# Kernel tuning notes

Hardware: AMD Instinct MI355X
Metric: run time of the kernel (lower is better)

## Reference

```python
import jax, jax.numpy as jnp
import numpy as np

N_NODES = 50000
N_EDGES = 800000
D_NODE = 128
D_EDGE = 128
D_OUT = 256
HID = 256


def setup_inputs() -> dict:
    key = jax.random.key(0)
    ks = jax.random.split(key, 10)
    s1 = 1.0 / np.sqrt(D_NODE + D_EDGE)
    s2 = 1.0 / np.sqrt(HID)
    s3 = 1.0 / np.sqrt(D_NODE + HID)
    return {
        "x": jax.random.normal(ks[0], (N_NODES, D_NODE), dtype=jnp.float32),
        "edge_index": jax.random.randint(ks[1], (2, N_EDGES), 0, N_NODES, dtype=jnp.int64),
        "edge_attr": jax.random.normal(ks[2], (N_EDGES, D_EDGE), dtype=jnp.float32),
        "u": jax.random.normal(ks[3], (1, 64), dtype=jnp.float32),
        "batch": jnp.zeros((N_NODES,), dtype=jnp.int64),
        "w1a": jax.random.normal(ks[4], (D_NODE + D_EDGE, HID), dtype=jnp.float32) * s1,
        "b1a": jnp.zeros((HID,), dtype=jnp.float32),
        "w1b": jax.random.normal(ks[5], (HID, HID), dtype=jnp.float32) * s2,
        "b1b": jnp.zeros((HID,), dtype=jnp.float32),
        "w2a": jax.random.normal(ks[6], (D_NODE + HID, HID), dtype=jnp.float32) * s3,
        "b2a": jnp.zeros((HID,), dtype=jnp.float32),
        "w2b": jax.random.normal(ks[7], (HID, D_OUT), dtype=jnp.float32) * s2,
        "b2b": jnp.zeros((D_OUT,), dtype=jnp.float32),
    }


def reference(x, edge_index, edge_attr, u, batch, w1a, b1a, w1b, b1b, w2a, b2a, w2b, b2b):
    row, col = edge_index[0], edge_index[1]
    # edge-wise MLP: [E, D_NODE + D_EDGE] -> 256 -> 256
    h = jnp.concatenate([x[row], edge_attr], axis=1)
    h = jax.nn.elu(h @ w1a + b1a) @ w1b + b1b  # [E, 256]
    # scatter_mean over destination nodes (dim_size = N)
    n = x.shape[0]
    sums = jax.ops.segment_sum(h, col, num_segments=n)  # [N, 256]
    cnt = jax.ops.segment_sum(jnp.ones((h.shape[0],), h.dtype), col, num_segments=n)
    mean = sums / jnp.maximum(cnt, 1.0)[:, None]
    # node-wise MLP: [N, D_NODE + 256] -> 256 -> D_OUT
    z = jnp.concatenate([x, mean], axis=1)
    return jax.nn.elu(z @ w2a + b2a) @ w2b + b2b
```

## Files before the change

### kernel.cpp

```cpp
#include <hip/hip_runtime.h>
#include <hip/hip_bf16.h>

#define N_NODES 50000
#define N_EDGES 800000

typedef short s16x8 __attribute__((ext_vector_type(8)));
typedef short s16x4 __attribute__((ext_vector_type(4)));
typedef float f32x4 __attribute__((ext_vector_type(4)));

__device__ __forceinline__ unsigned short f2bf(float f) {
    union { float f; unsigned u; } v; v.f = f;
    unsigned r = v.u + 0x7fffu + ((v.u >> 16) & 1u);
    return (unsigned short)(r >> 16);
}

__device__ __forceinline__ float bf2f(unsigned short u) {
    union { unsigned u; float f; } v; v.u = ((unsigned)u) << 16;
    return v.f;
}

__device__ __forceinline__ s16x8 ld8(const unsigned short* p) {
    return *(const s16x8*)p;
}

__device__ __forceinline__ float elu(float h) {
    return h > 0.0f ? h : (__expf(h) - 1.0f);
}

__global__ void wconv_kernel(const float* __restrict__ src,
                             unsigned short* __restrict__ dst,
                             int K, int N) {
    int idx = blockIdx.x * 256 + threadIdx.x;
    if (idx >= K * N) return;
    int n = idx / K;
    int k = idx - n * K;
    dst[idx] = f2bf(src[k * N + n]);
}

__global__ void hist_kernel(const int* __restrict__ ei, int* __restrict__ hist) {
    int e = blockIdx.x * 256 + threadIdx.x;
    if (e < N_EDGES) atomicAdd(&hist[ei[N_EDGES + e]], 1);
}

__global__ void scan_kernel(const int* __restrict__ hist, int* __restrict__ cursor) {
    __shared__ int tmp[1024];
    __shared__ int carryS;
    const int t = threadIdx.x;
    if (t == 0) carryS = 0;
    __syncthreads();
    for (int base = 0; base < N_NODES; base += 4096) {
        int i = base + t * 4;
        int4 v = {0, 0, 0, 0};
        if (i + 3 < N_NODES) v = *(const int4*)&hist[i];
        else {
            v.x = (i + 0 < N_NODES) ? hist[i + 0] : 0;
            v.y = (i + 1 < N_NODES) ? hist[i + 1] : 0;
            v.z = (i + 2 < N_NODES) ? hist[i + 2] : 0;
            v.w = (i + 3 < N_NODES) ? hist[i + 3] : 0;
        }
        int s = v.x + v.y + v.z + v.w;
        tmp[t] = s;
        __syncthreads();
        for (int off = 1; off < 1024; off <<= 1) {
            int add = (t >= off) ? tmp[t - off] : 0;
            __syncthreads();
            tmp[t] += add;
            __syncthreads();
        }
        int incl = tmp[t];
        int excl0 = carryS + incl - s;
        if (i     < N_NODES) cursor[i]     = excl0;
        if (i + 1 < N_NODES) cursor[i + 1] = excl0 + v.x;
        if (i + 2 < N_NODES) cursor[i + 2] = excl0 + v.x + v.y;
        if (i + 3 < N_NODES) cursor[i + 3] = excl0 + v.x + v.y + v.z;
        __syncthreads();
        if (t == 1023) carryS += incl;
        __syncthreads();
    }
}

__global__ void scatter_kernel(const int* __restrict__ ei, int* __restrict__ cursor,
                               int* __restrict__ sidx) {
    int e = blockIdx.x * 256 + threadIdx.x;
    if (e >= N_EDGES) return;
    int c = ei[N_EDGES + e];
    int p = atomicAdd(&cursor[c], 1);
    sidx[p] = e;
}

#define EP 264

__global__ __launch_bounds__(256, 4) void edge_kernel(
    const float* __restrict__ x, const int* __restrict__ ei,
    const float* __restrict__ ea, const int* __restrict__ sidx,
    const float* __restrict__ b1a,
    const unsigned short* __restrict__ w1aT,
    float* __restrict__ sums)
{
    __shared__ unsigned short lA[64 * EP];
    __shared__ int lrow[64];
    __shared__ int lcol[64];
    __shared__ int lidx[64];
    __shared__ unsigned char segstart[64];
    const int t = threadIdx.x;
    const int e0 = blockIdx.x * 64;

    if (t < 64) {
        int idx = sidx[e0 + t];
        lidx[t] = idx;
        lrow[t] = ei[idx];
        lcol[t] = ei[N_EDGES + idx];
    }
    __syncthreads();
    if (t < 64) segstart[t] = (t == 0) ? 1 : (lcol[t] != lcol[t - 1]);

    const f32x4* x4 = (const f32x4*)x;
    const f32x4* ea4 = (const f32x4*)ea;
#pragma unroll
    for (int i = 0; i < 8; i++) {
        int idx = i * 256 + t, r = idx >> 5, c4 = idx & 31;
        f32x4 v = x4[lrow[r] * 32 + c4];
        s16x4 b = { (short)f2bf(v.x), (short)f2bf(v.y), (short)f2bf(v.z), (short)f2bf(v.w) };
        *(s16x4*)&lA[r * EP + c4 * 4] = b;
    }
#pragma unroll
    for (int i = 0; i < 8; i++) {
        int idx = i * 256 + t, r = idx >> 5, c4 = idx & 31;
        f32x4 v = ea4[lidx[r] * 32 + c4];
        s16x4 b = { (short)f2bf(v.x), (short)f2bf(v.y), (short)f2bf(v.z), (short)f2bf(v.w) };
        *(s16x4*)&lA[r * EP + 128 + c4 * 4] = b;
    }
    __syncthreads();

    const int wv = t >> 6, lane = t & 63;
    const int quad = lane >> 4, l15 = lane & 15;

    f32x4 acc[4][4];
#pragma unroll
    for (int m = 0; m < 4; m++)
#pragma unroll
        for (int n = 0; n < 4; n++)
            acc[m][n] = (f32x4){0.f, 0.f, 0.f, 0.f};

    for (int kk = 0; kk < 8; kk++) {
        s16x8 a[4], b[4];
#pragma unroll
        for (int m = 0; m < 4; m++)
            a[m] = *(const s16x8*)&lA[(m * 16 + l15) * EP + kk * 32 + quad * 8];
#pragma unroll
        for (int n = 0; n < 4; n++)
            b[n] = ld8(&w1aT[(wv * 64 + n * 16 + l15) * 256 + kk * 32 + quad * 8]);
#pragma unroll
        for (int m = 0; m < 4; m++)
#pragma unroll
            for (int n = 0; n < 4; n++)
                acc[m][n] = __builtin_amdgcn_mfma_f32_16x16x32_bf16(a[m], b[n], acc[m][n], 0, 0, 0);
    }

    __syncthreads();

#pragma unroll
    for (int m = 0; m < 4; m++)
#pragma unroll
        for (int n = 0; n < 4; n++) {
            int col = wv * 64 + n * 16 + l15;
            float bias = b1a[col];
#pragma unroll
            for (int v = 0; v < 4; v++) {
                int row = m * 16 + quad * 4 + v;
                float h = elu(acc[m][n][v] + bias);
                lA[row * EP + col] = f2bf(h);
            }
        }
    __syncthreads();

    float s = 0.f;
    for (int r = 0; r < 64; r++) {
        if (r > 0 && segstart[r]) {
            atomicAdd(&sums[lcol[r - 1] * 256 + t], s);
            s = 0.f;
        }
        s += bf2f(lA[r * EP + t]);
    }
    atomicAdd(&sums[lcol[63] * 256 + t], s);
}

#define NP 392

__global__ __launch_bounds__(256, 3) void node_kernel(
    const float* __restrict__ x, const float* __restrict__ sums,
    const int* __restrict__ hist,
    const float* __restrict__ b1b, const float* __restrict__ b2a,
    const float* __restrict__ b2b,
    const unsigned short* __restrict__ w1bT, const unsigned short* __restrict__ w2aT,
    const unsigned short* __restrict__ w2bT,
    float* __restrict__ out)
{
    __shared__ unsigned short lZ[64 * NP];
    __shared__ float linv[64];
    __shared__ unsigned char lpos[64];
    const int t = threadIdx.x;
    const int n0 = blockIdx.x * 64;

    if (t < 64) {
        int c = 0;
        if (n0 + t < N_NODES) c = hist[n0 + t];
        lpos[t] = (c > 0);
        linv[t] = 1.0f / fmaxf((float)c, 1.0f);
    }
    __syncthreads();

#pragma unroll
    for (int i = 0; i < 8; i++) {
        int idx = i * 256 + t, r = idx >> 5, c4 = idx & 31;
        int node = n0 + r;
        f32x4 v = {0.f, 0.f, 0.f, 0.f};
        if (node < N_NODES) v = ((const f32x4*)x)[node * 32 + c4];
        s16x4 b = { (short)f2bf(v.x), (short)f2bf(v.y), (short)f2bf(v.z), (short)f2bf(v.w) };
        *(s16x4*)&lZ[r * NP + c4 * 4] = b;
    }
#pragma unroll
    for (int i = 0; i < 16; i++) {
        int idx = i * 256 + t, r = idx >> 6, c4 = idx & 63;
        int node = n0 + r;
        f32x4 v = {0.f, 0.f, 0.f, 0.f};
        if (node < N_NODES) v = ((const f32x4*)sums)[node * 64 + c4];
        float sc = linv[r];
        s16x4 b = { (short)f2bf(v.x * sc), (short)f2bf(v.y * sc),
                    (short)f2bf(v.z * sc), (short)f2bf(v.w * sc) };
        *(s16x4*)&lZ[r * NP + 128 + c4 * 4] = b;
    }
    __syncthreads();

    const int wv = t >> 6, lane = t & 63;
    const int quad = lane >> 4, l15 = lane & 15;

    f32x4 acc[4][4];
#pragma unroll
    for (int m = 0; m < 4; m++)
#pragma unroll
        for (int n = 0; n < 4; n++)
            acc[m][n] = (f32x4){0.f, 0.f, 0.f, 0.f};

    for (int kk = 0; kk < 8; kk++) {
        s16x8 a[4], b[4];
#pragma unroll
        for (int m = 0; m < 4; m++)
            a[m] = *(const s16x8*)&lZ[(m * 16 + l15) * NP + 128 + kk * 32 + quad * 8];
#pragma unroll
        for (int n = 0; n < 4; n++)
            b[n] = ld8(&w1bT[(wv * 64 + n * 16 + l15) * 256 + kk * 32 + quad * 8]);
#pragma unroll
        for (int m = 0; m < 4; m++)
#pragma unroll
            for (int n = 0; n < 4; n++)
                acc[m][n] = __builtin_amdgcn_mfma_f32_16x16x32_bf16(a[m], b[n], acc[m][n], 0, 0, 0);
    }
    __syncthreads();

#pragma unroll
    for (int m = 0; m < 4; m++)
#pragma unroll
        for (int n = 0; n < 4; n++) {
            int col = wv * 64 + n * 16 + l15;
            float bias = b1b[col];
#pragma unroll
            for (int v = 0; v < 4; v++) {
                int row = m * 16 + quad * 4 + v;
                float h = acc[m][n][v] + (lpos[row] ? bias : 0.f);
                lZ[row * NP + 128 + col] = f2bf(h);
            }
            acc[m][n] = (f32x4){0.f, 0.f, 0.f, 0.f};
        }
    __syncthreads();

    for (int kk = 0; kk < 12; kk++) {
        s16x8 a[4], b[4];
#pragma unroll
        for (int m = 0; m < 4; m++)
            a[m] = *(const s16x8*)&lZ[(m * 16 + l15) * NP + kk * 32 + quad * 8];
#pragma unroll
        for (int n = 0; n < 4; n++)
            b[n] = ld8(&w2aT[(wv * 64 + n * 16 + l15) * 384 + kk * 32 + quad * 8]);
#pragma unroll
        for (int m = 0; m < 4; m++)
#pragma unroll
            for (int n = 0; n < 4; n++)
                acc[m][n] = __builtin_amdgcn_mfma_f32_16x16x32_bf16(a[m], b[n], acc[m][n], 0, 0, 0);
    }
    __syncthreads();

#pragma unroll
    for (int m = 0; m < 4; m++)
#pragma unroll
        for (int n = 0; n < 4; n++) {
            int col = wv * 64 + n * 16 + l15;
            float bias = b2a[col];
#pragma unroll
            for (int v = 0; v < 4; v++) {
                int row = m * 16 + quad * 4 + v;
                float h = elu(acc[m][n][v] + bias);
                lZ[row * NP + col] = f2bf(h);
            }
            acc[m][n] = (f32x4){0.f, 0.f, 0.f, 0.f};
        }
    __syncthreads();

    for (int kk = 0; kk < 8; kk++) {
        s16x8 a[4], b[4];
#pragma unroll
        for (int m = 0; m < 4; m++)
            a[m] = *(const s16x8*)&lZ[(m * 16 + l15) * NP + kk * 32 + quad * 8];
#pragma unroll
        for (int n = 0; n < 4; n++)
            b[n] = ld8(&w2bT[(wv * 64 + n * 16 + l15) * 256 + kk * 32 + quad * 8]);
#pragma unroll
        for (int m = 0; m < 4; m++)
#pragma unroll
            for (int n = 0; n < 4; n++)
                acc[m][n] = __builtin_amdgcn_mfma_f32_16x16x32_bf16(a[m], b[n], acc[m][n], 0, 0, 0);
    }

#pragma unroll
    for (int m = 0; m < 4; m++)
#pragma unroll
        for (int n = 0; n < 4; n++) {
            int col = wv * 64 + n * 16 + l15;
            float bias = b2b[col];
#pragma unroll
            for (int v = 0; v < 4; v++) {
                int row = m * 16 + quad * 4 + v;
                int node = n0 + row;
                if (node < N_NODES)
                    out[node * 256 + col] = acc[m][n][v] + bias;
            }
        }
}

#define WS_SUMS   0u
#define WS_HIST   51200000u
#define WS_ZERO_BYTES 51400000u
#define WS_CURSOR 51400000u
#define WS_SIDX   51600000u
#define WS_W1A    54800000u
#define WS_W1B    54931072u
#define WS_W2A    55062144u
#define WS_W2B    55258752u

extern "C" void kernel_launch(void* const* d_in, const int* in_sizes, int n_in,
                              void* d_out, int out_size, void* d_ws, size_t ws_size,
                              hipStream_t stream) {
    const float* x   = (const float*)d_in[0];
    const int*   ei  = (const int*)d_in[1];
    const float* ea  = (const float*)d_in[2];
    const float* w1a = (const float*)d_in[5];
    const float* b1a = (const float*)d_in[6];
    const float* w1b = (const float*)d_in[7];
    const float* b1b = (const float*)d_in[8];
    const float* w2a = (const float*)d_in[9];
    const float* b2a = (const float*)d_in[10];
    const float* w2b = (const float*)d_in[11];
    const float* b2b = (const float*)d_in[12];
    float* out = (float*)d_out;

    char* ws = (char*)d_ws;
    float* sums = (float*)(ws + WS_SUMS);
    int* hist   = (int*)(ws + WS_HIST);
    int* cursor = (int*)(ws + WS_CURSOR);
    int* sidx   = (int*)(ws + WS_SIDX);
    unsigned short* w1aT = (unsigned short*)(ws + WS_W1A);
    unsigned short* w1bT = (unsigned short*)(ws + WS_W1B);
    unsigned short* w2aT = (unsigned short*)(ws + WS_W2A);
    unsigned short* w2bT = (unsigned short*)(ws + WS_W2B);

    hipMemsetAsync(d_ws, 0, WS_ZERO_BYTES, stream);

    wconv_kernel<<<(256 * 256 + 255) / 256, 256, 0, stream>>>(w1a, w1aT, 256, 256);
    wconv_kernel<<<(256 * 256 + 255) / 256, 256, 0, stream>>>(w1b, w1bT, 256, 256);
    wconv_kernel<<<(384 * 256 + 255) / 256, 256, 0, stream>>>(w2a, w2aT, 384, 256);
    wconv_kernel<<<(256 * 256 + 255) / 256, 256, 0, stream>>>(w2b, w2bT, 256, 256);

    hist_kernel<<<(N_EDGES + 255) / 256, 256, 0, stream>>>(ei, hist);
    scan_kernel<<<1, 1024, 0, stream>>>(hist, cursor);
    scatter_kernel<<<(N_EDGES + 255) / 256, 256, 0, stream>>>(ei, cursor, sidx);

    edge_kernel<<<N_EDGES / 64, 256, 0, stream>>>(x, ei, ea, sidx, b1a, w1aT, sums);

    node_kernel<<<(N_NODES + 63) / 64, 256, 0, stream>>>(x, sums, hist, b1b, b2a, b2b,
                                                         w1bT, w2aT, w2bT, out);
}
```

Before: 977.3 us.

## Reduce edge segments in registers, warp-shuffle scan, packed bf16 conversion

The edge kernel epilogue now applies bias+ELU in the MFMA accumulators and reduces rows belonging to each destination segment directly in registers via masked adds and cross-lane shuffles, removing the LDS write/readback and two barriers. Segment ids are computed with ballot/popcount. The single-block scan is rewritten to per-thread chunks with a wave-shuffle prefix instead of a barrier-heavy Hillis-Steele loop over many iterations. Float-to-bf16 conversions use the hardware packed convert instruction; the per-segment loop adds compare/select work proportional to segment count.

```diff
diff --git a/kernel.cpp b/kernel.cpp
--- a/kernel.cpp
+++ b/kernel.cpp
@@ -7,6 +7,7 @@
 typedef short s16x8 __attribute__((ext_vector_type(8)));
 typedef short s16x4 __attribute__((ext_vector_type(4)));
 typedef float f32x4 __attribute__((ext_vector_type(4)));
+typedef unsigned int u32x2 __attribute__((ext_vector_type(2)));
 
 __device__ __forceinline__ unsigned short f2bf(float f) {
     union { float f; unsigned u; } v; v.f = f;
@@ -14,9 +15,10 @@
     return (unsigned short)(r >> 16);
 }
 
-__device__ __forceinline__ float bf2f(unsigned short u) {
-    union { unsigned u; float f; } v; v.u = ((unsigned)u) << 16;
-    return v.f;
+__device__ __forceinline__ unsigned cvt_pk_bf16(float a, float b) {
+    unsigned r;
+    asm("v_cvt_pk_bf16_f32 %0, %1, %2" : "=v"(r) : "v"(a), "v"(b));
+    return r;
 }
 
 __device__ __forceinline__ s16x8 ld8(const unsigned short* p) {
@@ -43,39 +45,56 @@
 }
 
 __global__ void scan_kernel(const int* __restrict__ hist, int* __restrict__ cursor) {
-    __shared__ int tmp[1024];
-    __shared__ int carryS;
+    __shared__ int wsum[16];
     const int t = threadIdx.x;
-    if (t == 0) carryS = 0;
-    __syncthreads();
-    for (int base = 0; base < N_NODES; base += 4096) {
-        int i = base + t * 4;
-        int4 v = {0, 0, 0, 0};
-        if (i + 3 < N_NODES) v = *(const int4*)&hist[i];
-        else {
-            v.x = (i + 0 < N_NODES) ? hist[i + 0] : 0;
-            v.y = (i + 1 < N_NODES) ? hist[i + 1] : 0;
-            v.z = (i + 2 < N_NODES) ? hist[i + 2] : 0;
-            v.w = (i + 3 < N_NODES) ? hist[i + 3] : 0;
-        }
-        int s = v.x + v.y + v.z + v.w;
-        tmp[t] = s;
-        __syncthreads();
-        for (int off = 1; off < 1024; off <<= 1) {
-            int add = (t >= off) ? tmp[t - off] : 0;
-            __syncthreads();
-            tmp[t] += add;
-            __syncthreads();
-        }
-        int incl = tmp[t];
-        int excl0 = carryS + incl - s;
-        if (i     < N_NODES) cursor[i]     = excl0;
-        if (i + 1 < N_NODES) cursor[i + 1] = excl0 + v.x;
-        if (i + 2 < N_NODES) cursor[i + 2] = excl0 + v.x + v.y;
-        if (i + 3 < N_NODES) cursor[i + 3] = excl0 + v.x + v.y + v.z;
-        __syncthreads();
-        if (t == 1023) carryS += incl;
-        __syncthreads();
+    const int lane = t & 63, wv = t >> 6;
+    const int CHUNK = 52;
+    const int base = t * CHUNK;
+
+    int s = 0;
+    for (int i = 0; i < CHUNK; i += 4) {
+        int idx = base + i;
+        if (idx + 3 < N_NODES) {
+            int4 v = *(const int4*)&hist[idx];
+            s += v.x + v.y + v.z + v.w;
+        } else {
+#pragma unroll
+            for (int j = 0; j < 4; j++)
+                if (idx + j < N_NODES) s += hist[idx + j];
+        }
+    }
+    int incl = s;
+#pragma unroll
+    for (int off = 1; off < 64; off <<= 1) {
+        int o = __shfl_up(incl, off);
+        if (lane >= off) incl += o;
+    }
+    if (lane == 63) wsum[wv] = incl;
+    __syncthreads();
+    if (t == 0) {
+        int c = 0;
+#pragma unroll
+        for (int w = 0; w < 16; w++) { int v = wsum[w]; wsum[w] = c; c += v; }
+    }
+    __syncthreads();
+    int excl = wsum[wv] + (incl - s);
+
+    for (int i = 0; i < CHUNK; i += 4) {
+        int idx = base + i;
+        if (idx + 3 < N_NODES) {
+            int4 v = *(const int4*)&hist[idx];
+            int4 o;
+            o.x = excl;
+            o.y = o.x + v.x;
+            o.z = o.y + v.y;
+            o.w = o.z + v.z;
+            *(int4*)&cursor[idx] = o;
+            excl = o.w + v.w;
+        } else {
+#pragma unroll
+            for (int j = 0; j < 4; j++)
+                if (idx + j < N_NODES) { cursor[idx + j] = excl; excl += hist[idx + j]; }
+        }
     }
 }
 
@@ -99,20 +118,29 @@
 {
     __shared__ unsigned short lA[64 * EP];
     __shared__ int lrow[64];
-    __shared__ int lcol[64];
     __shared__ int lidx[64];
-    __shared__ unsigned char segstart[64];
+    __shared__ int lsegcol[64];
+    __shared__ unsigned char lsegid[64] __attribute__((aligned(4)));
+    __shared__ int lnseg;
     const int t = threadIdx.x;
     const int e0 = blockIdx.x * 64;
 
     if (t < 64) {
         int idx = sidx[e0 + t];
+        int r = ei[idx];
+        int c = ei[N_EDGES + idx];
         lidx[t] = idx;
-        lrow[t] = ei[idx];
-        lcol[t] = ei[N_EDGES + idx];
-    }
-    __syncthreads();
-    if (t < 64) segstart[t] = (t == 0) ? 1 : (lcol[t] != lcol[t - 1]);
+        lrow[t] = r;
+        int cprev = __shfl_up(c, 1);
+        int flag = (t == 0 || c != cprev) ? 1 : 0;
+        unsigned long long m = __ballot(flag != 0);
+        unsigned long long lm = (2ULL << t) - 1ULL;
+        int sid = __popcll(m & lm) - 1;
+        lsegid[t] = (unsigned char)sid;
+        if (flag) lsegcol[sid] = c;
+        if (t == 63) lnseg = __popcll(m);
+    }
+    __syncthreads();
 
     const f32x4* x4 = (const f32x4*)x;
     const f32x4* ea4 = (const f32x4*)ea;
@@ -120,15 +148,15 @@
     for (int i = 0; i < 8; i++) {
         int idx = i * 256 + t, r = idx >> 5, c4 = idx & 31;
         f32x4 v = x4[lrow[r] * 32 + c4];
-        s16x4 b = { (short)f2bf(v.x), (short)f2bf(v.y), (short)f2bf(v.z), (short)f2bf(v.w) };
-        *(s16x4*)&lA[r * EP + c4 * 4] = b;
+        u32x2 b = { cvt_pk_bf16(v.x, v.y), cvt_pk_bf16(v.z, v.w) };
+        *(u32x2*)&lA[r * EP + c4 * 4] = b;
     }
 #pragma unroll
     for (int i = 0; i < 8; i++) {
         int idx = i * 256 + t, r = idx >> 5, c4 = idx & 31;
         f32x4 v = ea4[lidx[r] * 32 + c4];
-        s16x4 b = { (short)f2bf(v.x), (short)f2bf(v.y), (short)f2bf(v.z), (short)f2bf(v.w) };
-        *(s16x4*)&lA[r * EP + 128 + c4 * 4] = b;
+        u32x2 b = { cvt_pk_bf16(v.x, v.y), cvt_pk_bf16(v.z, v.w) };
+        *(u32x2*)&lA[r * EP + 128 + c4 * 4] = b;
     }
     __syncthreads();
 
@@ -157,32 +185,44 @@
                 acc[m][n] = __builtin_amdgcn_mfma_f32_16x16x32_bf16(a[m], b[n], acc[m][n], 0, 0, 0);
     }
 
-    __syncthreads();
-
-#pragma unroll
-    for (int m = 0; m < 4; m++)
-#pragma unroll
-        for (int n = 0; n < 4; n++) {
-            int col = wv * 64 + n * 16 + l15;
-            float bias = b1a[col];
+#pragma unroll
+    for (int n = 0; n < 4; n++) {
+        float bias = b1a[wv * 64 + n * 16 + l15];
+#pragma unroll
+        for (int m = 0; m < 4; m++)
+#pragma unroll
+            for (int v = 0; v < 4; v++)
+                acc[m][n][v] = elu(acc[m][n][v] + bias);
+    }
+
+    unsigned gm[4];
+#pragma unroll
+    for (int m = 0; m < 4; m++)
+        gm[m] = *(const unsigned*)&lsegid[m * 16 + quad * 4];
+
+    const int ns = lnseg;
+    const int ocol = wv * 64 + quad * 16 + l15;
+    for (int s = 0; s < ns; s++) {
+        float p0 = 0.f, p1 = 0.f, p2 = 0.f, p3 = 0.f;
+#pragma unroll
+        for (int m = 0; m < 4; m++) {
 #pragma unroll
             for (int v = 0; v < 4; v++) {
-                int row = m * 16 + quad * 4 + v;
-                float h = elu(acc[m][n][v] + bias);
-                lA[row * EP + col] = f2bf(h);
+                if (((gm[m] >> (8 * v)) & 255u) == (unsigned)s) {
+                    p0 += acc[m][0][v];
+                    p1 += acc[m][1][v];
+                    p2 += acc[m][2][v];
+                    p3 += acc[m][3][v];
+                }
             }
         }
-    __syncthreads();
-
-    float s = 0.f;
-    for (int r = 0; r < 64; r++) {
-        if (r > 0 && segstart[r]) {
-            atomicAdd(&sums[lcol[r - 1] * 256 + t], s);
-            s = 0.f;
-        }
-        s += bf2f(lA[r * EP + t]);
-    }
-    atomicAdd(&sums[lcol[63] * 256 + t], s);
+        p0 += __shfl_xor(p0, 16); p0 += __shfl_xor(p0, 32);
+        p1 += __shfl_xor(p1, 16); p1 += __shfl_xor(p1, 32);
+        p2 += __shfl_xor(p2, 16); p2 += __shfl_xor(p2, 32);
+        p3 += __shfl_xor(p3, 16); p3 += __shfl_xor(p3, 32);
+        float val = (quad == 0) ? p0 : (quad == 1) ? p1 : ((quad == 2) ? p2 : p3);
+        atomicAdd(&sums[lsegcol[s] * 256 + ocol], val);
+    }
 }
 
 #define NP 392
@@ -216,8 +256,8 @@
         int node = n0 + r;
         f32x4 v = {0.f, 0.f, 0.f, 0.f};
         if (node < N_NODES) v = ((const f32x4*)x)[node * 32 + c4];
-        s16x4 b = { (short)f2bf(v.x), (short)f2bf(v.y), (short)f2bf(v.z), (short)f2bf(v.w) };
-        *(s16x4*)&lZ[r * NP + c4 * 4] = b;
+        u32x2 b = { cvt_pk_bf16(v.x, v.y), cvt_pk_bf16(v.z, v.w) };
+        *(u32x2*)&lZ[r * NP + c4 * 4] = b;
     }
 #pragma unroll
     for (int i = 0; i < 16; i++) {
@@ -226,9 +266,8 @@
         f32x4 v = {0.f, 0.f, 0.f, 0.f};
         if (node < N_NODES) v = ((const f32x4*)sums)[node * 64 + c4];
         float sc = linv[r];
-        s16x4 b = { (short)f2bf(v.x * sc), (short)f2bf(v.y * sc),
-                    (short)f2bf(v.z * sc), (short)f2bf(v.w * sc) };
-        *(s16x4*)&lZ[r * NP + 128 + c4 * 4] = b;
+        u32x2 b = { cvt_pk_bf16(v.x * sc, v.y * sc), cvt_pk_bf16(v.z * sc, v.w * sc) };
+        *(u32x2*)&lZ[r * NP + 128 + c4 * 4] = b;
     }
     __syncthreads();
 
```

Measured after the change: 976.7 us. Within noise of the previous version (-0.1%).
